# Kernel optimization log

Measured on AMD Instinct MI355X. Metric: run time of the kernel, lower is better.

Reference implementation:

```python
import jax, jax.numpy as jnp
import numpy as np

N_POWER_ITERS = 10  # torch spectral_norm power-iteration approximation of sigma_max

def _spectral_normalize(W):
    # Power iteration for largest singular value; u, v are treated as constants
    # w.r.t. gradients (matches torch.nn.utils.parametrizations.spectral_norm).
    u = jnp.ones((W.shape[0],), W.dtype) / jnp.sqrt(jnp.asarray(W.shape[0], W.dtype))
    def body(u, _):
        v = W.T @ u
        v = v / (jnp.linalg.norm(v) + 1e-12)
        u = W @ v
        u = u / (jnp.linalg.norm(u) + 1e-12)
        return u, None
    u, _ = jax.lax.scan(body, u, None, length=N_POWER_ITERS)
    u = jax.lax.stop_gradient(u)
    v = W.T @ u
    v = jax.lax.stop_gradient(v / (jnp.linalg.norm(v) + 1e-12))
    sigma = u @ (W @ v)
    return W / sigma

def setup_inputs() -> dict:
    key = jax.random.key(0)
    k1, k2, k3, k4 = jax.random.split(key, 4)
    B, T, D_in, H, D_out = 32, 1024, 1024, 1024, 1024
    x = jax.random.normal(k1, (B, T, D_in), dtype=jnp.float32)
    # nn.Linear weight shape: [out_features, in_features]
    W_A = jax.random.normal(k2, (H, H), dtype=jnp.float32) * (1.0 / np.sqrt(H))
    W_B = jax.random.normal(k3, (H, D_in), dtype=jnp.float32) * (1.0 / np.sqrt(D_in))
    W_C = jax.random.normal(k4, (D_out, H), dtype=jnp.float32) * (1.0 / np.sqrt(H))
    return {"x": x, "W_A": W_A, "W_B": W_B, "W_C": W_C}

def reference(x, W_A, W_B, W_C):
    A = _spectral_normalize(W_A)   # [H, H]
    Bw = _spectral_normalize(W_B)  # [H, D_in]
    C = _spectral_normalize(W_C)   # [D_out, H]
    # Precompute input projection for all timesteps: [B, T, H]
    xb = jnp.einsum('bti,hi->bth', x, Bw)
    h0 = jnp.zeros((x.shape[0], A.shape[0]), x.dtype)
    def step(h, xb_t):
        h = h @ A.T + xb_t   # h_t = A h_{t-1} + B x_t
        return h, h
    _, hs = jax.lax.scan(step, h0, jnp.swapaxes(xb, 0, 1))  # [T, B, H]
    hs = jnp.swapaxes(hs, 0, 1)                              # [B, T, H]
    ys = jnp.einsum('bth,oh->bto', hs, C)                    # y_t = C h_t
    return ys, hs
```

## Files before the change

kernel.cpp:

```cpp
#include <hip/hip_runtime.h>
#include <hip/hip_fp16.h>
#include <stdint.h>
#include <math.h>


typedef unsigned short us;
typedef float  floatx4 __attribute__((ext_vector_type(4)));
typedef short  shortx8 __attribute__((ext_vector_type(8)));

#define HDIM 1024
#define MALL 32768
#define PNB  32

__device__ __forceinline__ us f2bf(float f) {
  union { float f; unsigned u; } v; v.f = f;
  unsigned u = v.u;
  return (us)((u + 0x7FFFu + ((u >> 16) & 1u)) >> 16);
}
__device__ __forceinline__ float bf2f(us h) {
  union { float f; unsigned u; } v; v.u = ((unsigned)h) << 16;
  return v.f;
}

__device__ __forceinline__ float bsum32(float t) {
  #pragma unroll
  for (int o = 16; o > 0; o >>= 1) t += __shfl_xor(t, o, 32);
  return t;
}

__device__ __forceinline__ float gload(const float* p) {
  return __hip_atomic_load((float*)p, __ATOMIC_RELAXED, __HIP_MEMORY_SCOPE_AGENT);
}
__device__ __forceinline__ float2 gload2(const float* p) {
  unsigned long long r = __hip_atomic_load((unsigned long long*)p,
                                           __ATOMIC_RELAXED, __HIP_MEMORY_SCOPE_AGENT);
  union { unsigned long long u; float2 f; } v; v.u = r; return v.f;
}
__device__ __forceinline__ void gstore(float* p, float x) {
  __hip_atomic_store(p, x, __ATOMIC_RELAXED, __HIP_MEMORY_SCOPE_AGENT);
}

__device__ __forceinline__ void gbar(int* flag, int b, int phase) {
  const int tid = threadIdx.x;
  __syncthreads();
  if (tid == 0)
    __hip_atomic_store(flag + b, phase, __ATOMIC_RELAXED, __HIP_MEMORY_SCOPE_AGENT);
  if (tid < PNB) {
    for (;;) {
      int f = __hip_atomic_load(flag + tid, __ATOMIC_RELAXED, __HIP_MEMORY_SCOPE_AGENT);
      if (__ballot(f < phase) == 0ULL) break;
      __builtin_amdgcn_s_sleep(2);
    }
  }
  __syncthreads();
}

__global__ void k_power(const float* __restrict__ WA, const float* __restrict__ WB,
                        const float* __restrict__ WC,
                        float* __restrict__ uu, float* __restrict__ vv,
                        float* __restrict__ part, int* __restrict__ bar) {
  const int m = blockIdx.y, b = blockIdx.x, tid = threadIdx.x;
  const float* W = m == 0 ? WA : (m == 1 ? WB : WC);
  float* um = uu + m * 1024;
  float* vm = vv + m * 1024;
  float* PV = part + m * 1024;
  float* PU = part + m * 1024 + 512;
  int* flag = bar + m * PNB;

  __shared__ __align__(16) float sh[1024];
  __shared__ __align__(16) float red[512];
  __shared__ float bc;

  const int il = tid & 31, jp = tid >> 5;
  const int jr = tid >> 4, ip = tid & 15;

  int ph = 0;
  for (int it = 0; it <= 10; ++it) {
    if (it == 0) {
      ((float2*)sh)[tid] = make_float2(0.03125f, 0.03125f);
      __syncthreads();
    } else {
      if (tid < 32) {
        float t = bsum32(gload(PU + (it - 1) * 32 + tid));
        if (tid == 0) bc = rsqrtf(t + 1e-24f);
      }
      __syncthreads();
      float su = bc;
      float2 u2 = gload2(um + tid * 2);
      ((float2*)sh)[tid] = make_float2(u2.x * su, u2.y * su);
      __syncthreads();
    }

    {
      const int col = b * 32 + il;
      const float* Wp = W + (size_t)(jp * 64) * 1024 + col;
      const float* up = sh + jp * 64;
      float a0 = 0.f, a1 = 0.f, a2 = 0.f, a3 = 0.f, a4 = 0.f, a5 = 0.f, a6 = 0.f, a7 = 0.f;
      #pragma unroll
      for (int j = 0; j < 64; j += 8) {
        a0 = fmaf(Wp[(size_t)(j + 0) * 1024], up[j + 0], a0);
        a1 = fmaf(Wp[(size_t)(j + 1) * 1024], up[j + 1], a1);
        a2 = fmaf(Wp[(size_t)(j + 2) * 1024], up[j + 2], a2);
        a3 = fmaf(Wp[(size_t)(j + 3) * 1024], up[j + 3], a3);
        a4 = fmaf(Wp[(size_t)(j + 4) * 1024], up[j + 4], a4);
        a5 = fmaf(Wp[(size_t)(j + 5) * 1024], up[j + 5], a5);
        a6 = fmaf(Wp[(size_t)(j + 6) * 1024], up[j + 6], a6);
        a7 = fmaf(Wp[(size_t)(j + 7) * 1024], up[j + 7], a7);
      }
      red[tid] = ((a0 + a1) + (a2 + a3)) + ((a4 + a5) + (a6 + a7));
      __syncthreads();
      if (tid < 32) {
        float s = 0.f;
        #pragma unroll
        for (int g = 0; g < 16; ++g) s += red[tid + 32 * g];
        gstore(vm + b * 32 + tid, s);
        float t = bsum32(s * s);
        if (tid == 0) gstore(PV + it * 32 + b, t);
      }
    }
    if (it == 10) break;
    gbar(flag, b, ++ph);

    if (tid < 32) {
      float t = bsum32(gload(PV + it * 32 + tid));
      if (tid == 0) bc = rsqrtf(t + 1e-24f);
    }
    __syncthreads();
    {
      float sv = bc;
      float2 v2 = gload2(vm + tid * 2);
      ((float2*)sh)[tid] = make_float2(v2.x * sv, v2.y * sv);
    }
    __syncthreads();

    {
      const int row = b * 32 + jr;
      const float* Wr = W + (size_t)row * 1024;
      float b0 = 0.f, b1 = 0.f, b2 = 0.f, b3 = 0.f, b4 = 0.f, b5 = 0.f, b6 = 0.f, b7 = 0.f;
      #pragma unroll
      for (int k = 0; k < 64; k += 8) {
        b0 = fmaf(Wr[ip + 16 * (k + 0)], sh[ip + 16 * (k + 0)], b0);
        b1 = fmaf(Wr[ip + 16 * (k + 1)], sh[ip + 16 * (k + 1)], b1);
        b2 = fmaf(Wr[ip + 16 * (k + 2)], sh[ip + 16 * (k + 2)], b2);
        b3 = fmaf(Wr[ip + 16 * (k + 3)], sh[ip + 16 * (k + 3)], b3);
        b4 = fmaf(Wr[ip + 16 * (k + 4)], sh[ip + 16 * (k + 4)], b4);
        b5 = fmaf(Wr[ip + 16 * (k + 5)], sh[ip + 16 * (k + 5)], b5);
        b6 = fmaf(Wr[ip + 16 * (k + 6)], sh[ip + 16 * (k + 6)], b6);
        b7 = fmaf(Wr[ip + 16 * (k + 7)], sh[ip + 16 * (k + 7)], b7);
      }
      float acc = ((b0 + b1) + (b2 + b3)) + ((b4 + b5) + (b6 + b7));
      acc += __shfl_down(acc, 8, 16);
      acc += __shfl_down(acc, 4, 16);
      acc += __shfl_down(acc, 2, 16);
      acc += __shfl_down(acc, 1, 16);
      if (ip == 0) { gstore(um + row, acc); red[jr] = acc * acc; }
      __syncthreads();
      if (tid < 32) {
        float t = bsum32(red[tid]);
        if (tid == 0) gstore(PU + it * 32 + b, t);
      }
    }
    gbar(flag, b, ++ph);
  }
}

__global__ void k_cast_mats(const float* __restrict__ WA, const float* __restrict__ WB,
                            const float* __restrict__ WC, const float* __restrict__ part,
                            us* __restrict__ dst) {
  __shared__ float bcs;
  const int m = (int)(((unsigned)blockIdx.x * 256u) >> 18);
  if (threadIdx.x < 32) {
    float t = bsum32(part[m * 1024 + 10 * 32 + threadIdx.x]);
    if (threadIdx.x == 0) bcs = rsqrtf(t + 1e-24f);
  }
  __syncthreads();
  float rs = bcs;
  int idx = blockIdx.x * 256 + threadIdx.x;
  const float* W = m == 0 ? WA : (m == 1 ? WB : WC);
  float4 v = ((const float4*)W)[idx & 262143];
  unsigned lo = f2bf(v.x * rs) | ((unsigned)f2bf(v.y * rs) << 16);
  unsigned hi = f2bf(v.z * rs) | ((unsigned)f2bf(v.w * rs) << 16);
  ((uint2*)dst)[idx] = make_uint2(lo, hi);
}

__global__ void k_cast_x(const float* __restrict__ src, us* __restrict__ dst, int n4) {
  int idx = blockIdx.x * 256 + threadIdx.x;
  int stride = gridDim.x * 256;
  for (; idx < n4; idx += stride) {
    float4 v = ((const float4*)src)[idx];
    unsigned lo = f2bf(v.x) | ((unsigned)f2bf(v.y) << 16);
    unsigned hi = f2bf(v.z) | ((unsigned)f2bf(v.w) << 16);
    ((uint2*)dst)[idx] = make_uint2(lo, hi);
  }
}

__global__ void k_transpose(const us* __restrict__ src, us* __restrict__ dst) {
  __shared__ us t[32][33];
  int bx = blockIdx.x * 32, by = blockIdx.y * 32;
  int tx = threadIdx.x & 31, ty = threadIdx.x >> 5;
  for (int r = ty; r < 32; r += 8)
    t[r][tx] = src[(size_t)(by + r) * 1024 + bx + tx];
  __syncthreads();
  for (int r = ty; r < 32; r += 8)
    dst[(size_t)(bx + r) * 1024 + by + tx] = t[tx][r];
}

template <int TILE>
__global__ __launch_bounds__(256, 3)
void k_gemm(const us* __restrict__ Abf, const us* __restrict__ Bmat,
            const us* __restrict__ AccP,
            float* __restrict__ Out32, us* __restrict__ Out16, us* __restrict__ OutH,
            us* __restrict__ Copy16,
            int M, int stride_log, int delta_a, int delta_acc, int delta_copy,
            int accmode, int zero_aop) {
  constexpr int BK = 64;
  constexpr int WT = TILE / 2;
  constexpr int NT = WT / 16;
  constexpr int QA = TILE / 32;

  __shared__ us ldsA[TILE * BK];
  __shared__ us ldsB[TILE * BK];

  const int tid = threadIdx.x;
  const int wave = tid >> 6, lane = tid & 63;
  const int wr = wave >> 1, wc = wave & 1;
  const int lr = lane & 15, g = lane >> 4;
  const int m0 = blockIdx.x * TILE, n0 = blockIdx.y * TILE;

  const int cnt_log = 10 - stride_log;
  const int cnt_mask = (1 << cnt_log) - 1;
  auto rowC = [&](int m) -> int {
    int j = m & cnt_mask, b = m >> cnt_log;
    return (b << 10) + (((j + 1) << stride_log) - 1);
  };

  floatx4 acc[NT][NT];
  if (accmode == 0) {
    #pragma unroll
    for (int i = 0; i < NT; ++i)
      #pragma unroll
      for (int j = 0; j < NT; ++j) acc[i][j] = (floatx4)(0.0f);
  } else {
    #pragma unroll
    for (int ii = 0; ii < NT; ++ii) {
      #pragma unroll
      for (int r = 0; r < 4; ++r) {
        int m = m0 + wr * WT + ii * 16 + g * 4 + r;
        if (m >= M) m = M - 1;
        size_t rowoff = (size_t)(rowC(m) - delta_acc) * HDIM;
        #pragma unroll
        for (int jj = 0; jj < NT; ++jj) {
          int col = n0 + wc * WT + jj * 16 + lr;
          us raw = AccP[rowoff + col];
          acc[ii][jj][r] = (accmode == 2) ? bf2f(raw)
                                          : __half2float(*(const __half*)&raw);
        }
      }
    }
  }

  if (!zero_aop) {
    size_t abase[QA], bbase[QA];
    #pragma unroll
    for (int q = 0; q < QA; ++q) {
      int ch = tid + q * 256;
      int i = ch >> 3;
      int c = (ch & 7) ^ ((i >> 1) & 7);
      int m = m0 + i; if (m >= M) m = M - 1;
      abase[q] = (size_t)(rowC(m) - delta_a) * HDIM + c * 8;
      bbase[q] = (size_t)(n0 + i) * HDIM + c * 8;
    }
    for (int k0 = 0; k0 < HDIM; k0 += BK) {
      __syncthreads();
      #pragma unroll
      for (int q = 0; q < QA; ++q) {
        __builtin_amdgcn_global_load_lds(
            (const __attribute__((address_space(1))) void*)(Abf + abase[q] + k0),
            (__attribute__((address_space(3))) void*)(ldsA + (wave * 64 + q * 256) * 8),
            16, 0, 0);
        __builtin_amdgcn_global_load_lds(
            (const __attribute__((address_space(1))) void*)(Bmat + bbase[q] + k0),
            (__attribute__((address_space(3))) void*)(ldsB + (wave * 64 + q * 256) * 8),
            16, 0, 0);
      }
      __syncthreads();
      #pragma unroll
      for (int kk = 0; kk < 2; ++kk) {
        shortx8 af[NT], bfv[NT];
        #pragma unroll
        for (int ii = 0; ii < NT; ++ii) {
          int ra = wr * WT + ii * 16 + lr;
          af[ii] = *(const shortx8*)(ldsA + ra * BK + (((kk * 4 + g) ^ ((ra >> 1) & 7)) * 8));
          int rb = wc * WT + ii * 16 + lr;
          bfv[ii] = *(const shortx8*)(ldsB + rb * BK + (((kk * 4 + g) ^ ((rb >> 1) & 7)) * 8));
        }
        #pragma unroll
        for (int ii = 0; ii < NT; ++ii)
          #pragma unroll
          for (int jj = 0; jj < NT; ++jj)
            acc[ii][jj] = __builtin_amdgcn_mfma_f32_16x16x32_bf16(af[ii], bfv[jj], acc[ii][jj], 0, 0, 0);
      }
    }
  }

  #pragma unroll
  for (int ii = 0; ii < NT; ++ii) {
    #pragma unroll
    for (int r = 0; r < 4; ++r) {
      int m = m0 + wr * WT + ii * 16 + g * 4 + r;
      if (m >= M) continue;
      size_t rowoff = (size_t)rowC(m) * HDIM;
      #pragma unroll
      for (int jj = 0; jj < NT; ++jj) {
        int col = n0 + wc * WT + jj * 16 + lr;
        float v = acc[ii][jj][r];
        if (Copy16) {
          us pv = zero_aop ? (us)0 : Abf[rowoff + col];
          Copy16[(size_t)(rowC(m) - delta_copy) * HDIM + col] = pv;
        }
        if (Out32) Out32[rowoff + col] = v;
        if (Out16) Out16[rowoff + col] = f2bf(v);
        if (OutH) {
          __half hv = __float2half(v);
          OutH[rowoff + col] = *(const us*)&hv;
        }
      }
    }
  }
}

extern "C" void kernel_launch(void* const* d_in, const int* in_sizes, int n_in,
                              void* d_out, int out_size, void* d_ws, size_t ws_size,
                              hipStream_t stream) {
  const float* x  = (const float*)d_in[0];
  const float* WA = (const float*)d_in[1];
  const float* WB = (const float*)d_in[2];
  const float* WC = (const float*)d_in[3];

  float* ys = (float*)d_out;
  float* U  = ys + (size_t)MALL * HDIM;
  us* U16 = (us*)U;

  char* wsb = (char*)d_ws;
  int*   bar  = (int*)(wsb);
  float* uu   = (float*)(wsb + 4096);
  float* vv   = (float*)(wsb + 20480);
  float* part = (float*)(wsb + 32768);
  us* An = (us*)(wsb + 65536);
  us* Bn = An + 1048576;
  us* Cn = Bn + 1048576;
  us* PT = Cn + 1048576;
  us* Ppow[9];
  Ppow[0] = An;
  for (int d = 1; d <= 8; ++d) Ppow[d] = PT + (size_t)d * 1048576;
  us* Xbf  = (us*)(wsb + 25231360);
  us* Uh   = Xbf;
  us* U0bf = Xbf + (size_t)MALL * HDIM;
  us* Ubf  = U0bf + (size_t)MALL * HDIM;
  if (ws_size < 226643968ULL) return;

  auto gemm = [&](int tile, const us* A, const us* B, const us* accP,
                  float* o32, us* o16, us* oH, us* cp16,
                  int M, int slog, int da, int dacc, int dcp, int am, int za) {
    dim3 grid((M + tile - 1) / tile, HDIM / tile);
    if (tile == 128)
      k_gemm<128><<<grid, 256, 0, stream>>>(A, B, accP, o32, o16, oH, cp16, M, slog, da, dacc, dcp, am, za);
    else
      k_gemm<64><<<grid, 256, 0, stream>>>(A, B, accP, o32, o16, oH, cp16, M, slog, da, dacc, dcp, am, za);
  };

  hipMemsetAsync(bar, 0, 3 * PNB * sizeof(int), stream);
  k_power<<<dim3(PNB, 3), 512, 0, stream>>>(WA, WB, WC, uu, vv, part, bar);

  k_cast_mats<<<dim3(3072), 256, 0, stream>>>(WA, WB, WC, part, An);
  k_cast_x<<<dim3(8192), 256, 0, stream>>>(x, Xbf, 8388608);

  for (int d = 1; d <= 8; ++d) {
    k_transpose<<<dim3(32, 32), 256, 0, stream>>>(Ppow[d - 1], PT);
    gemm(64, Ppow[d - 1], PT, nullptr, nullptr, Ppow[d], nullptr, nullptr,
         1024, 0, 0, 0, 0, 0, 0);
  }

  gemm(128, Xbf, Bn, nullptr, nullptr, U0bf, nullptr, nullptr, MALL, 0, 0, 0, 0, 0, 0);

  for (int d = 0; d <= 8; ++d) {
    int M = MALL >> (d + 1);
    const us* srcA = (d == 0) ? U0bf : Ubf;
    const us* accP = (d == 0) ? U0bf : Uh;
    int am = (d == 0) ? 2 : 3;
    gemm(M >= 2048 ? 128 : 64, srcA, Ppow[d], accP, nullptr, Ubf, Uh, nullptr,
         M, d + 1, 1 << d, 0, 0, am, 0);
  }

  {
    us* PP2[2] = {U16, Ubf};
    for (int idx = 0; idx <= 9; ++idx) {
      int d = 9 - idx;
      int M = MALL >> (d + 1);
      const us* srcA = idx ? PP2[(idx - 1) & 1] : nullptr;
      us* dst = PP2[idx & 1];
      const us* accP = (d == 0) ? U0bf : Uh;
      int am = (d == 0) ? 2 : 3;
      gemm(M >= 2048 ? 128 : 64, srcA, Ppow[d], accP,
           nullptr, dst, nullptr, dst,
           M, d + 1, 0, 1 << d, 1 << d, am, idx == 0 ? 1 : 0);
    }
  }

  gemm(128, Ubf, An, U0bf, U, U0bf, nullptr, nullptr, MALL, 0, 0, 0, 0, 2, 0);

  gemm(128, U0bf, Cn, nullptr, ys, nullptr, nullptr, nullptr, MALL, 0, 0, 0, 0, 0, 0);
}
```

Baseline: 1.338 ms.

## Add 256x256-tile bf16 MFMA GEMM with 4-stage LDS pipeline for large GEMMs

```diff
diff --git a/kernel.cpp b/kernel.cpp
--- a/kernel.cpp
+++ b/kernel.cpp
@@ -324,6 +324,107 @@
           __half hv = __float2half(v);
           OutH[rowoff + col] = *(const us*)&hv;
         }
+      }
+    }
+  }
+}
+
+#define NK256 32
+
+__global__ __launch_bounds__(512, 2)
+void k_gemm256(const us* __restrict__ Abf, const us* __restrict__ Bmat,
+               const us* __restrict__ AccP,
+               float* __restrict__ Out32, us* __restrict__ Out16) {
+  __shared__ __align__(16) us lds[4][2][8192];
+
+  const int tid = threadIdx.x;
+  const int wave = tid >> 6, lane = tid & 63;
+  const int wr = wave >> 2, wc = wave & 3;
+  const int lr = lane & 15, g = lane >> 4;
+
+  const int nwg = gridDim.x * gridDim.y;
+  int lid = blockIdx.x + blockIdx.y * gridDim.x;
+  int s = (lid & 7) * (nwg >> 3) + (lid >> 3);
+  const int m0 = (s >> 2) * 256, n0 = (s & 3) * 256;
+
+  const us* srcA[2]; const us* srcB[2]; int ldst[2];
+  #pragma unroll
+  for (int q = 0; q < 2; ++q) {
+    int kappa = q * 512 + tid;
+    int l = kappa >> 3, phi = kappa & 7, psi = phi ^ (l & 7);
+    int row = 2 * l + (psi >> 2), c = psi & 3;
+    srcA[q] = Abf + (size_t)(m0 + row) * HDIM + c * 8;
+    srcB[q] = Bmat + (size_t)(n0 + row) * HDIM + c * 8;
+    ldst[q] = (q * 512 + wave * 64) * 8;
+  }
+
+  auto stage = [&](int kt) {
+    const int bi = kt & 3;
+    const int ko = kt * 32;
+    #pragma unroll
+    for (int q = 0; q < 2; ++q) {
+      __builtin_amdgcn_global_load_lds(
+          (const __attribute__((address_space(1))) void*)(srcA[q] + ko),
+          (__attribute__((address_space(3))) void*)(&lds[bi][0][0] + ldst[q]), 16, 0, 0);
+      __builtin_amdgcn_global_load_lds(
+          (const __attribute__((address_space(1))) void*)(srcB[q] + ko),
+          (__attribute__((address_space(3))) void*)(&lds[bi][1][0] + ldst[q]), 16, 0, 0);
+    }
+  };
+
+  floatx4 acc[8][4];
+  #pragma unroll
+  for (int i = 0; i < 8; ++i)
+    #pragma unroll
+    for (int j = 0; j < 4; ++j) acc[i][j] = (floatx4)(0.0f);
+
+  stage(0); stage(1); stage(2);
+  asm volatile("s_waitcnt vmcnt(8)" ::: "memory");
+
+  for (int kt = 0; kt < NK256; ++kt) {
+    asm volatile("" ::: "memory");
+    __builtin_amdgcn_s_barrier();
+    asm volatile("" ::: "memory");
+    if (kt + 3 < NK256) stage(kt + 3);
+    const int bi = kt & 3;
+
+    shortx8 bq[4];
+    #pragma unroll
+    for (int jj = 0; jj < 4; ++jj) {
+      int rb = wc * 64 + jj * 16 + lr;
+      int phi = ((((rb & 1) << 2) | g) ^ ((rb >> 1) & 7));
+      bq[jj] = *(const shortx8*)(&lds[bi][1][(rb >> 1) * 64 + phi * 8]);
+    }
+    __builtin_amdgcn_s_setprio(1);
+    #pragma unroll
+    for (int ii = 0; ii < 8; ++ii) {
+      int ra = wr * 128 + ii * 16 + lr;
+      int phi = ((((ra & 1) << 2) | g) ^ ((ra >> 1) & 7));
+      shortx8 aq = *(const shortx8*)(&lds[bi][0][(ra >> 1) * 64 + phi * 8]);
+      #pragma unroll
+      for (int jj = 0; jj < 4; ++jj)
+        acc[ii][jj] = __builtin_amdgcn_mfma_f32_16x16x32_bf16(aq, bq[jj], acc[ii][jj], 0, 0, 0);
+    }
+    __builtin_amdgcn_s_setprio(0);
+
+    if (kt < NK256 - 3)       asm volatile("s_waitcnt vmcnt(8)" ::: "memory");
+    else if (kt == NK256 - 3) asm volatile("s_waitcnt vmcnt(4)" ::: "memory");
+    else if (kt == NK256 - 2) asm volatile("s_waitcnt vmcnt(0)" ::: "memory");
+  }
+
+  #pragma unroll
+  for (int ii = 0; ii < 8; ++ii) {
+    #pragma unroll
+    for (int r = 0; r < 4; ++r) {
+      int mrow = m0 + wr * 128 + ii * 16 + g * 4 + r;
+      size_t rowoff = (size_t)mrow * HDIM;
+      #pragma unroll
+      for (int jj = 0; jj < 4; ++jj) {
+        int col = n0 + wc * 64 + jj * 16 + lr;
+        float v = acc[ii][jj][r];
+        if (AccP) v += bf2f(AccP[rowoff + col]);
+        if (Out32) Out32[rowoff + col] = v;
+        if (Out16) Out16[rowoff + col] = f2bf(v);
       }
     }
   }
@@ -368,6 +469,9 @@
     else
       k_gemm<64><<<grid, 256, 0, stream>>>(A, B, accP, o32, o16, oH, cp16, M, slog, da, dacc, dcp, am, za);
   };
+  auto gemm256 = [&](const us* A, const us* B, const us* accP, float* o32, us* o16) {
+    k_gemm256<<<dim3(MALL / 256, 4), 512, 0, stream>>>(A, B, accP, o32, o16);
+  };
 
   hipMemsetAsync(bar, 0, 3 * PNB * sizeof(int), stream);
   k_power<<<dim3(PNB, 3), 512, 0, stream>>>(WA, WB, WC, uu, vv, part, bar);
@@ -381,7 +485,7 @@
          1024, 0, 0, 0, 0, 0, 0);
   }
 
-  gemm(128, Xbf, Bn, nullptr, nullptr, U0bf, nullptr, nullptr, MALL, 0, 0, 0, 0, 0, 0);
+  gemm256(Xbf, Bn, nullptr, nullptr, U0bf);
 
   for (int d = 0; d <= 8; ++d) {
     int M = MALL >> (d + 1);
@@ -407,7 +511,7 @@
     }
   }
 
-  gemm(128, Ubf, An, U0bf, U, U0bf, nullptr, nullptr, MALL, 0, 0, 0, 0, 2, 0);
-
-  gemm(128, U0bf, Cn, nullptr, ys, nullptr, nullptr, nullptr, MALL, 0, 0, 0, 0, 0, 0);
-}
+  gemm256(Ubf, An, U0bf, U, U0bf);
+
+  gemm256(U0bf, Cn, nullptr, ys, nullptr);
+}
```

Result: no change. 1.335 ms (-0.2%).
